# Optimization experiments

Measured on AMD Instinct MI355X. Metric: run time of the kernel, lower is better.

## Reference

```python
import jax, jax.numpy as jnp
import numpy as np

EPS = 1e-8
TAU = 0.2
IOU_THR = 0.5
NEG = -1e9
N, C, H, D_FG, D_CLS = 8192, 1024, 256, 64, 128


def setup_inputs() -> dict:
    key = jax.random.key(0)
    ks = jax.random.split(key, 11)
    def lin(k, fan_in, fan_out):
        return jax.random.normal(k, (fan_in, fan_out), jnp.float32) / np.sqrt(fan_in)
    return {
        "roi_feats": jax.random.normal(ks[0], (N, C), jnp.float32),
        "labels": jax.random.randint(ks[1], (N,), 0, 21, jnp.int32).astype(jnp.int64),
        "ious": jax.random.uniform(ks[2], (N,), jnp.float32),
        "fg_w1": lin(ks[3], C, H), "fg_b1": jnp.zeros((H,), jnp.float32),
        "fg_w2": lin(ks[4], H, D_FG), "fg_b2": jnp.zeros((D_FG,), jnp.float32),
        "cls_w1": lin(ks[5], C, H), "cls_b1": jnp.zeros((H,), jnp.float32),
        "cls_w2": lin(ks[6], H, D_CLS), "cls_b2": jnp.zeros((D_CLS,), jnp.float32),
    }


def _project_normalize(x, w1, b1, w2, b2):
    h = jax.nn.relu(x @ w1 + b1)
    z = h @ w2 + b2
    norm = jnp.maximum(jnp.linalg.norm(z, axis=1, keepdims=True), EPS)
    return z / norm


def _forward(roi_feats, labels, ious, fg_w1, fg_b1, fg_w2, fg_b2, cls_w1, cls_b1, cls_w2, cls_b2):
    n = roi_feats.shape[0]
    z_fg = _project_normalize(roi_feats, fg_w1, fg_b1, fg_w2, fg_b2)
    z_cls = _project_normalize(roi_feats, cls_w1, cls_b1, cls_w2, cls_b2)

    ignore = labels == -1
    fg = (labels > 0) & ~ignore
    iou_weight = jnp.where(ious > IOU_THR, ious, 0.0)
    eye = jnp.eye(n, dtype=bool)

    # ---- fg/bg contrastive (bg_as_negatives_only=True) ----
    sim_fg = (z_fg @ z_fg.T) / TAU                       # [N,N]
    exp_sim = jnp.exp(sim_fg)
    denom = jnp.sum(exp_sim * (~eye).astype(jnp.float32), axis=1)
    pos = (fg & ~ignore)[None, :] & ~eye                 # positives: fg columns, no self
    n_pos = jnp.sum(pos, axis=1)
    numer = jnp.sum(exp_sim * pos.astype(jnp.float32), axis=1)
    # original computes den = denom + EPS then -log((numer+EPS)/(den+EPS))
    loss_i = -jnp.log((numer + EPS) / (denom + 2.0 * EPS))
    valid = (fg & ~ignore) & (n_pos > 0)
    w = iou_weight * valid.astype(jnp.float32)
    loss_fg_bg = jnp.sum(w * loss_i) / (jnp.sum(w) + EPS)

    # ---- class supervised contrastive ----
    sim_cls = (z_cls @ z_cls.T) / TAU
    sim_masked = jnp.where(eye, NEG, sim_cls)
    log_denom = jax.nn.logsumexp(sim_masked, axis=1)     # [N]
    log_p = jnp.where(eye, NEG, sim_cls - log_denom[:, None])
    # pos_mask keeps diagonal (as in original): same label, col not ignore, col label != 0
    posc = (labels[None, :] == labels[:, None]) & (~ignore)[None, :] & (labels[None, :] != 0)
    n_posc = jnp.sum(posc, axis=1).astype(jnp.float32)
    sum_log_p = jnp.sum(log_p * posc.astype(jnp.float32), axis=1)
    valid_c = (fg & ~ignore) & (n_posc > 0) & jnp.isfinite(log_denom)
    Lzi = jnp.where(valid_c, -sum_log_p / (n_posc + EPS), 0.0)
    wc = iou_weight * valid_c.astype(jnp.float32)
    loss_supcon = jnp.sum(wc * Lzi) / (jnp.sum(wc) + EPS)

    return jnp.stack([loss_fg_bg, loss_supcon])


def reference(roi_feats, labels, ious, fg_w1, fg_b1, fg_w2, fg_b2, cls_w1, cls_b1, cls_w2, cls_b2):
    return _forward(roi_feats, labels, ious, fg_w1, fg_b1, fg_w2, fg_b2, cls_w1, cls_b1, cls_w2, cls_b2)
```

## Files before the change

kernel.cpp:

```cpp
#include <hip/hip_runtime.h>


typedef __attribute__((ext_vector_type(8))) short bs8;
typedef __attribute__((ext_vector_type(4))) float f4;

#define MFMA_BF16(a, b, c) __builtin_amdgcn_mfma_f32_16x16x32_bf16((a), (b), (c), 0, 0, 0)

#if defined(__has_builtin)
#if __has_builtin(__builtin_amdgcn_exp2f)
#define EXP2F(x) __builtin_amdgcn_exp2f(x)
#endif
#endif
#ifndef EXP2F
#define EXP2F(x) exp2f(x)
#endif

#define K_LOG2E 7.2134752044448170f

__device__ __forceinline__ unsigned short f2bf(float f) {
  unsigned int u = __float_as_uint(f);
  u = (u + 0x7fffu + ((u >> 16) & 1u)) >> 16;
  return (unsigned short)u;
}
__device__ __forceinline__ float bf2f(unsigned short s) {
  return __uint_as_float(((unsigned int)s) << 16);
}

constexpr size_t O_W1T  = 0;
constexpr size_t O_W2TF = 1048576;
constexpr size_t O_W2TC = 1081344;
constexpr size_t O_H    = 1146880;
constexpr size_t O_ZF   = 9535488;
constexpr size_t O_ZC   = 10584064;
constexpr size_t O_SCLS = 12681216;
constexpr size_t O_ROWD = 12697600;
constexpr size_t O_ROWN = 12730368;
constexpr size_t O_ROWS = 12763136;
constexpr size_t O_SCAL = 12795904;
constexpr size_t O_HIST = 12795920;
constexpr size_t O_NFG  = 12796048;
constexpr size_t O_CNT  = O_SCLS + 31 * 128 * 4;
constexpr int ZERO_WORDS = (int)((O_SCAL + 16 - O_SCLS) / 4);

__global__ void __launch_bounds__(256) prep_kernel(
    const float* __restrict__ fgw1, const float* __restrict__ clsw1,
    const float* __restrict__ fgw2, const float* __restrict__ clsw2,
    const int* __restrict__ labels,
    unsigned short* __restrict__ W1T, unsigned short* __restrict__ W2Tf,
    unsigned short* __restrict__ W2Tc,
    int* __restrict__ hist, int* __restrict__ nfg, float* __restrict__ zp) {
  const int b = blockIdx.x;
  const int t = threadIdx.x;

  if (b >= 141) {
    const int i = (b - 141) * 256 + t;
    if (i < ZERO_WORDS) zp[i] = 0.f;
    return;
  }
  if (b == 140) {
    __shared__ int sh[33];
    if (t < 33) sh[t] = 0;
    __syncthreads();
    for (int it = 0; it < 32; it++) {
      const int lab = labels[it * 256 + t];
      if (lab >= 0 && lab < 32) atomicAdd(&sh[lab], 1);
      if (lab > 0) atomicAdd(&sh[32], 1);
    }
    __syncthreads();
    if (t < 32) hist[t] = sh[t];
    if (t == 32) *nfg = sh[32];
    return;
  }
  int m, tb;
  if (b < 64)       { m = 0; tb = b; }
  else if (b < 128) { m = 1; tb = b - 64; }
  else if (b < 132) { m = 2; tb = b - 128; }
  else              { m = 3; tb = b - 132; }
  __shared__ float tile[64][65];
  const float* src;
  unsigned short* dst;
  int R, C;
  if (m == 0)      { src = fgw1;  dst = W1T;              R = 1024; C = 256; }
  else if (m == 1) { src = clsw1; dst = W1T + 256 * 1024; R = 1024; C = 256; }
  else if (m == 2) { src = fgw2;  dst = W2Tf;             R = 256;  C = 64;  }
  else             { src = clsw2; dst = W2Tc;             R = 256;  C = 128; }
  const int cT = C >> 6;
  const int r0 = (tb / cT) << 6, c0 = (tb % cT) << 6;
  {
    const int rr = t >> 4, cc = (t & 15) << 2;
#pragma unroll
    for (int i = 0; i < 4; i++) {
      float4 v = *(const float4*)(src + (size_t)(r0 + rr + i * 16) * C + c0 + cc);
      tile[rr + i * 16][cc] = v.x; tile[rr + i * 16][cc + 1] = v.y;
      tile[rr + i * 16][cc + 2] = v.z; tile[rr + i * 16][cc + 3] = v.w;
    }
  }
  __syncthreads();
  {
    const int dr = t >> 2, dc = (t & 3) << 4;
    bs8 o0, o1;
#pragma unroll
    for (int j = 0; j < 8; j++) o0[j] = (short)f2bf(tile[dc + j][dr]);
#pragma unroll
    for (int j = 0; j < 8; j++) o1[j] = (short)f2bf(tile[dc + 8 + j][dr]);
    unsigned short* dp = dst + (size_t)(c0 + dr) * R + r0 + dc;
    *(bs8*)dp = o0;
    *(bs8*)(dp + 8) = o1;
  }
}

__global__ void __launch_bounds__(512) gemm1_kernel(
    const float* __restrict__ X, const unsigned short* __restrict__ W1T,
    const float* __restrict__ b1f, const float* __restrict__ b1c,
    unsigned short* __restrict__ H) {
  __shared__ __align__(16) unsigned short lA[64 * 72];
  __shared__ __align__(16) unsigned short lB[128 * 72];
  const int t = threadIdx.x;
  const int w = t >> 6, lane = t & 63, ln = lane & 15, quad = lane >> 4;
  const int wr = (w & 3) * 16, wc = (w >> 2) * 64;
  const int m0 = blockIdx.x * 64, n0 = blockIdx.y * 128;

  const int ar = t >> 3, ac = (t & 7) * 8;
  const int br = t >> 2, bc = (t & 3) * 16;
  const float* xbase = X + (size_t)(m0 + ar) * 1024 + ac;
  const unsigned short* bbase = W1T + (size_t)(n0 + br) * 1024 + bc;

  float4 xa[2];
  bs8 xb[2];
#pragma unroll
  for (int i = 0; i < 2; i++) xa[i] = *(const float4*)(xbase + i * 4);
#pragma unroll
  for (int i = 0; i < 2; i++) xb[i] = *(const bs8*)(bbase + i * 8);

  f4 acc[4];
#pragma unroll
  for (int s = 0; s < 4; s++) acc[s] = (f4){0.f, 0.f, 0.f, 0.f};

  for (int ks = 0; ks < 16; ks++) {
    {
      bs8 av;
      av[0] = (short)f2bf(xa[0].x); av[1] = (short)f2bf(xa[0].y);
      av[2] = (short)f2bf(xa[0].z); av[3] = (short)f2bf(xa[0].w);
      av[4] = (short)f2bf(xa[1].x); av[5] = (short)f2bf(xa[1].y);
      av[6] = (short)f2bf(xa[1].z); av[7] = (short)f2bf(xa[1].w);
      *(bs8*)&lA[ar * 72 + ac] = av;
      unsigned short* bp = &lB[br * 72 + bc];
      *(bs8*)(bp) = xb[0];
      *(bs8*)(bp + 8) = xb[1];
    }
    __syncthreads();
    if (ks < 15) {
      const int k1 = (ks + 1) * 64;
#pragma unroll
      for (int i = 0; i < 2; i++) xa[i] = *(const float4*)(xbase + k1 + i * 4);
#pragma unroll
      for (int i = 0; i < 2; i++) xb[i] = *(const bs8*)(bbase + k1 + i * 8);
    }
#pragma unroll
    for (int kk = 0; kk < 2; kk++) {
      bs8 af = *(const bs8*)&lA[(wr + ln) * 72 + kk * 32 + quad * 8];
#pragma unroll
      for (int s = 0; s < 4; s++) {
        bs8 bf = *(const bs8*)&lB[(wc + s * 16 + ln) * 72 + kk * 32 + quad * 8];
        acc[s] = MFMA_BF16(af, bf, acc[s]);
      }
    }
    __syncthreads();
  }
#pragma unroll
  for (int s = 0; s < 4; s++) {
    const int n = n0 + wc + s * 16 + ln;
    const float b = (n < 256) ? b1f[n] : b1c[n - 256];
#pragma unroll
    for (int r = 0; r < 4; r++) {
      float v = fmaxf(acc[s][r] + b, 0.f);
      H[(size_t)(m0 + wr + quad * 4 + r) * 512 + n] = f2bf(v);
    }
  }
}

__global__ void __launch_bounds__(256) gemm2_kernel(
    const unsigned short* __restrict__ H,
    const unsigned short* __restrict__ W2Tf, const unsigned short* __restrict__ W2Tc,
    const float* __restrict__ b2f, const float* __restrict__ b2c,
    const int* __restrict__ labels,
    unsigned short* __restrict__ Zf, unsigned short* __restrict__ Zc,
    float* __restrict__ Scls) {
  __shared__ float sS[21 * 128];
  const int t = threadIdx.x;
  for (int i = t; i < 21 * 128; i += 256) sS[i] = 0.f;
  __syncthreads();

  const int w = t >> 6, lane = t & 63, ln = lane & 15, quad = lane >> 4;
  const int rw = blockIdx.x * 32 + (w & 1) * 16;

  if (w < 2) {
    const unsigned short* hrow = H + (size_t)(rw + ln) * 512;
    f4 acc[4];
#pragma unroll
    for (int s = 0; s < 4; s++) acc[s] = (f4){0.f, 0.f, 0.f, 0.f};
#pragma unroll
    for (int ks = 0; ks < 8; ks++) {
      bs8 af = *(const bs8*)(hrow + ks * 32 + quad * 8);
#pragma unroll
      for (int s = 0; s < 4; s++) {
        bs8 bf = *(const bs8*)(W2Tf + (size_t)(s * 16 + ln) * 256 + ks * 32 + quad * 8);
        acc[s] = MFMA_BF16(af, bf, acc[s]);
      }
    }
    float ss[4] = {0.f, 0.f, 0.f, 0.f};
#pragma unroll
    for (int s = 0; s < 4; s++) {
      float b = b2f[s * 16 + ln];
#pragma unroll
      for (int r = 0; r < 4; r++) {
        acc[s][r] += b;
        ss[r] = fmaf(acc[s][r], acc[s][r], ss[r]);
      }
    }
#pragma unroll
    for (int r = 0; r < 4; r++) {
#pragma unroll
      for (int off = 1; off < 16; off <<= 1) ss[r] += __shfl_xor(ss[r], off, 64);
      float sc = 1.f / fmaxf(sqrtf(ss[r]), 1e-8f);
#pragma unroll
      for (int s = 0; s < 4; s++)
        Zf[(size_t)(rw + quad * 4 + r) * 64 + s * 16 + ln] = f2bf(acc[s][r] * sc);
    }
  } else {
    const unsigned short* hrow = H + (size_t)(rw + ln) * 512 + 256;
    f4 acc[8];
#pragma unroll
    for (int s = 0; s < 8; s++) acc[s] = (f4){0.f, 0.f, 0.f, 0.f};
#pragma unroll
    for (int ks = 0; ks < 8; ks++) {
      bs8 af = *(const bs8*)(hrow + ks * 32 + quad * 8);
#pragma unroll
      for (int s = 0; s < 8; s++) {
        bs8 bf = *(const bs8*)(W2Tc + (size_t)(s * 16 + ln) * 256 + ks * 32 + quad * 8);
        acc[s] = MFMA_BF16(af, bf, acc[s]);
      }
    }
    float ss[4] = {0.f, 0.f, 0.f, 0.f};
#pragma unroll
    for (int s = 0; s < 8; s++) {
      float b = b2c[s * 16 + ln];
#pragma unroll
      for (int r = 0; r < 4; r++) {
        acc[s][r] += b;
        ss[r] = fmaf(acc[s][r], acc[s][r], ss[r]);
      }
    }
#pragma unroll
    for (int r = 0; r < 4; r++) {
#pragma unroll
      for (int off = 1; off < 16; off <<= 1) ss[r] += __shfl_xor(ss[r], off, 64);
      float sc = 1.f / fmaxf(sqrtf(ss[r]), 1e-8f);
      const int lab = labels[rw + quad * 4 + r];
#pragma unroll
      for (int s = 0; s < 8; s++) {
        const unsigned short us = f2bf(acc[s][r] * sc);
        Zc[(size_t)(rw + quad * 4 + r) * 128 + s * 16 + ln] = us;
        if (lab > 0 && lab < 21) atomicAdd(&sS[lab * 128 + s * 16 + ln], bf2f(us));
      }
    }
  }

  __syncthreads();
  for (int i = t; i < 20 * 128; i += 256) {
    const float v = sS[128 + i];
    if (v != 0.f) atomicAdd(&Scls[128 + i], v);
  }
}

__global__ void __launch_bounds__(256) sim2_kernel(
    const unsigned short* __restrict__ Zf, const unsigned short* __restrict__ Zc,
    const int* __restrict__ labels,
    float* __restrict__ rowD, float* __restrict__ rowN, float* __restrict__ rowS) {
  const int bi = blockIdx.x, y = blockIdx.y;
  const bool isfg = (y < 9);
  const int y2 = isfg ? y : y - 9;
  int dlo, dhi;
  if (y2 == 0)      { dlo = 0;      dhi = 3;      }
  else if (y2 < 8)  { dlo = y2 * 4; dhi = y2 * 4 + 3; }
  else              { dlo = 32;     dhi = 32; if (bi >= 32) return; }

  __shared__ __align__(16) char arena[19456];
  const int t = threadIdx.x;
  const int w = t >> 6, lane = t & 63, ln = lane & 15, quad = lane >> 4;
  const int rbase = bi * 128 + w * 32;

  if (isfg) {
    unsigned short* sZf = (unsigned short*)arena;
    float* sFg = (float*)(arena + 9216);
    float* sCol = (float*)(arena + 9472);

    bs8 afg[2][2];
    float fgr[2][4];
#pragma unroll
    for (int rs = 0; rs < 2; rs++) {
      const unsigned short* zf = Zf + (size_t)(rbase + rs * 16 + ln) * 64;
#pragma unroll
      for (int s = 0; s < 2; s++) afg[rs][s] = *(const bs8*)(zf + s * 32 + quad * 8);
#pragma unroll
      for (int r = 0; r < 4; r++)
        fgr[rs][r] = (labels[rbase + rs * 16 + quad * 4 + r] > 0) ? 1.f : 0.f;
    }

    float dacc[2][4] = {}, nacc[2][4] = {};

    for (int d = dlo; d <= dhi; d++) {
      const int bj = (bi + d) & 63;
      float cd[2][4] = {}, cn[2][4] = {};

#pragma unroll
      for (int ct = 0; ct < 2; ct++) {
        const int c0 = bj * 128 + ct * 64;
        __syncthreads();
#pragma unroll
        for (int i = 0; i < 2; i++) {
          int ch = t + i * 256;
          int j = ch >> 3, c8 = (ch & 7) * 8;
          *(bs8*)&sZf[j * 72 + c8] = *(const bs8*)(Zf + (size_t)(c0 + j) * 64 + c8);
        }
        if (t < 64) sFg[t] = (labels[c0 + t] > 0) ? 1.f : 0.f;
        __syncthreads();

#pragma unroll
        for (int s = 0; s < 4; s++) {
          const int lcol = s * 16 + ln;
          const float fgc = sFg[lcol];
          bs8 b0 = *(const bs8*)&sZf[lcol * 72 + quad * 8];
          bs8 b1 = *(const bs8*)&sZf[lcol * 72 + 32 + quad * 8];
#pragma unroll
          for (int rs = 0; rs < 2; rs++) {
            f4 c = {0.f, 0.f, 0.f, 0.f};
            c = MFMA_BF16(afg[rs][0], b0, c);
            c = MFMA_BF16(afg[rs][1], b1, c);
#pragma unroll
            for (int r = 0; r < 4; r++) {
              float e = EXP2F(c[r] * K_LOG2E);
              dacc[rs][r] += e;
              nacc[rs][r] = fmaf(fgc, e, nacc[rs][r]);
              cd[ct][s] += e;
              cn[ct][s] = fmaf(fgr[rs][r], e, cn[ct][s]);
            }
          }
        }
      }

      if (d != 0) {
#pragma unroll
        for (int ct = 0; ct < 2; ct++)
#pragma unroll
          for (int s = 0; s < 4; s++) {
            float dv = cd[ct][s], nv = cn[ct][s];
#pragma unroll
            for (int off = 16; off < 64; off <<= 1) {
              dv += __shfl_xor(dv, off, 64);
              nv += __shfl_xor(nv, off, 64);
            }
            if (quad == 0) {
              const int idx = (((w * 2 + ct) * 4 + s) * 16 + ln) * 2;
              sCol[idx] = dv;
              sCol[idx + 1] = nv;
            }
          }
        __syncthreads();
        if (t < 128) {
          const int ct = t >> 6, s = (t >> 4) & 3, lm = t & 15;
          float dv = 0.f, nv = 0.f;
#pragma unroll
          for (int ww = 0; ww < 4; ww++) {
            const int idx = (((ww * 2 + ct) * 4 + s) * 16 + lm) * 2;
            dv += sCol[idx];
            nv += sCol[idx + 1];
          }
          const int col = bj * 128 + t;
          atomicAdd(&rowD[col], dv);
          atomicAdd(&rowN[col], nv);
        }
      }
    }

#pragma unroll
    for (int rs = 0; rs < 2; rs++)
#pragma unroll
      for (int r = 0; r < 4; r++) {
        float dv = dacc[rs][r], nv = nacc[rs][r];
#pragma unroll
        for (int off = 1; off < 16; off <<= 1) {
          dv += __shfl_xor(dv, off, 64);
          nv += __shfl_xor(nv, off, 64);
        }
        if (ln == 0) {
          int row = rbase + rs * 16 + quad * 4 + r;
          atomicAdd(&rowD[row], dv);
          atomicAdd(&rowN[row], nv);
        }
      }
  } else {
    unsigned short* sZc = (unsigned short*)arena;
    float* sCol = (float*)(arena + 17408);

    bs8 acl[2][4];
#pragma unroll
    for (int rs = 0; rs < 2; rs++) {
      const unsigned short* zc = Zc + (size_t)(rbase + rs * 16 + ln) * 128;
#pragma unroll
      for (int s = 0; s < 4; s++) acl[rs][s] = *(const bs8*)(zc + s * 32 + quad * 8);
    }

    float sacc[2][4] = {};

    for (int d = dlo; d <= dhi; d++) {
      const int bj = (bi + d) & 63;
      float cs[2][4] = {};

#pragma unroll
      for (int ct = 0; ct < 2; ct++) {
        const int c0 = bj * 128 + ct * 64;
        __syncthreads();
#pragma unroll
        for (int i = 0; i < 4; i++) {
          int ch = t + i * 256;
          int j = ch >> 4, c8 = (ch & 15) * 8;
          *(bs8*)&sZc[j * 136 + c8] = *(const bs8*)(Zc + (size_t)(c0 + j) * 128 + c8);
        }
        __syncthreads();

#pragma unroll
        for (int s = 0; s < 4; s++) {
          const int lcol = s * 16 + ln;
          bs8 bc0 = *(const bs8*)&sZc[lcol * 136 + quad * 8];
          bs8 bc1 = *(const bs8*)&sZc[lcol * 136 + 32 + quad * 8];
          bs8 bc2 = *(const bs8*)&sZc[lcol * 136 + 64 + quad * 8];
          bs8 bc3 = *(const bs8*)&sZc[lcol * 136 + 96 + quad * 8];
#pragma unroll
          for (int rs = 0; rs < 2; rs++) {
            f4 c = {0.f, 0.f, 0.f, 0.f};
            c = MFMA_BF16(acl[rs][0], bc0, c);
            c = MFMA_BF16(acl[rs][1], bc1, c);
            c = MFMA_BF16(acl[rs][2], bc2, c);
            c = MFMA_BF16(acl[rs][3], bc3, c);
#pragma unroll
            for (int r = 0; r < 4; r++) {
              float e = EXP2F(c[r] * K_LOG2E);
              sacc[rs][r] += e;
              cs[ct][s] += e;
            }
          }
        }
      }

      if (d != 0) {
#pragma unroll
        for (int ct = 0; ct < 2; ct++)
#pragma unroll
          for (int s = 0; s < 4; s++) {
            float sv = cs[ct][s];
#pragma unroll
            for (int off = 16; off < 64; off <<= 1) sv += __shfl_xor(sv, off, 64);
            if (quad == 0) sCol[((w * 2 + ct) * 4 + s) * 16 + ln] = sv;
          }
        __syncthreads();
        if (t < 128) {
          const int ct = t >> 6, s = (t >> 4) & 3, lm = t & 15;
          float sv = 0.f;
#pragma unroll
          for (int ww = 0; ww < 4; ww++) sv += sCol[((ww * 2 + ct) * 4 + s) * 16 + lm];
          atomicAdd(&rowS[bj * 128 + t], sv);
        }
      }
    }

#pragma unroll
    for (int rs = 0; rs < 2; rs++)
#pragma unroll
      for (int r = 0; r < 4; r++) {
        float sv = sacc[rs][r];
#pragma unroll
        for (int off = 1; off < 16; off <<= 1) sv += __shfl_xor(sv, off, 64);
        if (ln == 0)
          atomicAdd(&rowS[rbase + rs * 16 + quad * 4 + r], sv);
      }
  }
}

__global__ void __launch_bounds__(256) finalize_kernel(
    const unsigned short* __restrict__ Zf, const unsigned short* __restrict__ Zc,
    const int* __restrict__ labels, const float* __restrict__ ious,
    const float* __restrict__ rowD, const float* __restrict__ rowN,
    const float* __restrict__ rowS, const float* __restrict__ Scls,
    const int* __restrict__ hist, const int* __restrict__ nfg,
    float* __restrict__ scal, unsigned int* __restrict__ cnt,
    float* __restrict__ out) {
  __shared__ float red[4][4];
  const int t = threadIdx.x, w = t >> 6, lane = t & 63;
  float aw0 = 0.f, al0 = 0.f, aw1 = 0.f, al1 = 0.f;
  const int NFG = *nfg;
  for (int it = 0; it < 16; it++) {
    const int i = it * 512 + blockIdx.x * 4 + w;
    const int lab = labels[i];
    if (lab > 0 && lab < 32) {
      const float iou = ious[i];
      const float iw = (iou > 0.5f) ? iou : 0.f;
      float dot = 0.f, ssq = 0.f;
#pragma unroll
      for (int p = 0; p < 2; p++) {
        const int k = lane + p * 64;
        const float z = bf2f(Zc[(size_t)i * 128 + k]);
        dot = fmaf(z, Scls[lab * 128 + k], dot);
        ssq = fmaf(z, z, ssq);
      }
      float zf = bf2f(Zf[(size_t)i * 64 + lane]);
      float ssqf = zf * zf;
#pragma unroll
      for (int off = 1; off < 64; off <<= 1) {
        dot += __shfl_xor(dot, off, 64);
        ssq += __shfl_xor(ssq, off, 64);
        ssqf += __shfl_xor(ssqf, off, 64);
      }
      if (lane == 0) {
        const float ef = EXP2F(K_LOG2E * ssqf);
        if (NFG - 1 > 0) {
          const float D = rowD[i] - ef;
          const float Nn = rowN[i] - ef;
          const float loss = logf(D + 2e-8f) - logf(Nn + 1e-8f);
          aw0 += iw;
          al0 += iw * loss;
        }
        const int npc = hist[lab];
        if (npc > 0) {
          const float S = rowS[i] - EXP2F(K_LOG2E * ssq);
          const float logden = logf(S);
          const float slp = (dot - ssq) * 5.0f - (float)(npc - 1) * logden - 1e9f;
          aw1 += iw;
          al1 += iw * (-slp / ((float)npc + 1e-8f));
        }
      }
    }
  }
  if (lane == 0) { red[w][0] = aw0; red[w][1] = al0; red[w][2] = aw1; red[w][3] = al1; }
  __syncthreads();
  if (t < 4) atomicAdd(&scal[t], red[0][t] + red[1][t] + red[2][t] + red[3][t]);
  __syncthreads();
  if (t == 0) {
    __threadfence();
    const unsigned int ticket = atomicAdd(cnt, 1u);
    if (ticket == gridDim.x - 1) {
      __threadfence();
      const float s0 = atomicAdd(&scal[0], 0.f);
      const float s1 = atomicAdd(&scal[1], 0.f);
      const float s2 = atomicAdd(&scal[2], 0.f);
      const float s3 = atomicAdd(&scal[3], 0.f);
      out[0] = s1 / (s0 + 1e-8f);
      out[1] = s3 / (s2 + 1e-8f);
    }
  }
}

extern "C" void kernel_launch(void* const* d_in, const int* in_sizes, int n_in,
                              void* d_out, int out_size, void* d_ws, size_t ws_size,
                              hipStream_t stream) {
  (void)in_sizes; (void)n_in; (void)out_size; (void)ws_size;
  const float* roi    = (const float*)d_in[0];
  const int*   labels = (const int*)d_in[1];
  const float* ious   = (const float*)d_in[2];
  const float* fgw1   = (const float*)d_in[3];
  const float* fgb1   = (const float*)d_in[4];
  const float* fgw2   = (const float*)d_in[5];
  const float* fgb2   = (const float*)d_in[6];
  const float* clsw1  = (const float*)d_in[7];
  const float* clsb1  = (const float*)d_in[8];
  const float* clsw2  = (const float*)d_in[9];
  const float* clsb2  = (const float*)d_in[10];

  char* ws = (char*)d_ws;
  unsigned short* W1T  = (unsigned short*)(ws + O_W1T);
  unsigned short* W2Tf = (unsigned short*)(ws + O_W2TF);
  unsigned short* W2Tc = (unsigned short*)(ws + O_W2TC);
  unsigned short* Hb   = (unsigned short*)(ws + O_H);
  unsigned short* Zf   = (unsigned short*)(ws + O_ZF);
  unsigned short* Zc   = (unsigned short*)(ws + O_ZC);
  float* Scls = (float*)(ws + O_SCLS);
  float* rowD = (float*)(ws + O_ROWD);
  float* rowN = (float*)(ws + O_ROWN);
  float* rowS = (float*)(ws + O_ROWS);
  float* scal = (float*)(ws + O_SCAL);
  unsigned int* cnt = (unsigned int*)(ws + O_CNT);
  int* hist = (int*)(ws + O_HIST);
  int* nfg  = (int*)(ws + O_NFG);
  float* out = (float*)d_out;

  hipLaunchKernelGGL(prep_kernel, dim3(254), dim3(256), 0, stream,
                     fgw1, clsw1, fgw2, clsw2, labels, W1T, W2Tf, W2Tc,
                     hist, nfg, (float*)(ws + O_SCLS));
  hipLaunchKernelGGL(gemm1_kernel, dim3(128, 4), dim3(512), 0, stream,
                     roi, W1T, fgb1, clsb1, Hb);
  hipLaunchKernelGGL(gemm2_kernel, dim3(256), dim3(256), 0, stream,
                     Hb, W2Tf, W2Tc, fgb2, clsb2, labels, Zf, Zc, Scls);
  hipLaunchKernelGGL(sim2_kernel, dim3(64, 18), dim3(256), 0, stream,
                     Zf, Zc, labels, rowD, rowN, rowS);
  hipLaunchKernelGGL(finalize_kernel, dim3(128), dim3(256), 0, stream,
                     Zf, Zc, labels, ious, rowD, rowN, rowS, Scls, hist, nfg,
                     scal, cnt, out);
}
```

Measured before the change: 201.6 us.

## Fuse fg and class similarity passes into one sim2 block per tile pair

Result: slower. 224.8 us (+11.5%).

```diff
diff --git a/kernel.cpp b/kernel.cpp
--- a/kernel.cpp
+++ b/kernel.cpp
@@ -278,213 +278,154 @@
     const int* __restrict__ labels,
     float* __restrict__ rowD, float* __restrict__ rowN, float* __restrict__ rowS) {
   const int bi = blockIdx.x, y = blockIdx.y;
-  const bool isfg = (y < 9);
-  const int y2 = isfg ? y : y - 9;
   int dlo, dhi;
-  if (y2 == 0)      { dlo = 0;      dhi = 3;      }
-  else if (y2 < 8)  { dlo = y2 * 4; dhi = y2 * 4 + 3; }
-  else              { dlo = 32;     dhi = 32; if (bi >= 32) return; }
-
-  __shared__ __align__(16) char arena[19456];
+  if (y < 16) { dlo = 2 * y; dhi = 2 * y + 1; }
+  else        { dlo = 32;    dhi = 32; if (bi >= 32) return; }
+
+  __shared__ __align__(16) unsigned short sZf[64 * 72];
+  __shared__ __align__(16) unsigned short sZc[64 * 136];
+  __shared__ float sFg[64];
+  __shared__ float sCol[4][2][4][16][3];
   const int t = threadIdx.x;
   const int w = t >> 6, lane = t & 63, ln = lane & 15, quad = lane >> 4;
   const int rbase = bi * 128 + w * 32;
 
-  if (isfg) {
-    unsigned short* sZf = (unsigned short*)arena;
-    float* sFg = (float*)(arena + 9216);
-    float* sCol = (float*)(arena + 9472);
-
-    bs8 afg[2][2];
-    float fgr[2][4];
-#pragma unroll
-    for (int rs = 0; rs < 2; rs++) {
-      const unsigned short* zf = Zf + (size_t)(rbase + rs * 16 + ln) * 64;
-#pragma unroll
-      for (int s = 0; s < 2; s++) afg[rs][s] = *(const bs8*)(zf + s * 32 + quad * 8);
-#pragma unroll
-      for (int r = 0; r < 4; r++)
-        fgr[rs][r] = (labels[rbase + rs * 16 + quad * 4 + r] > 0) ? 1.f : 0.f;
-    }
-
-    float dacc[2][4] = {}, nacc[2][4] = {};
-
-    for (int d = dlo; d <= dhi; d++) {
-      const int bj = (bi + d) & 63;
-      float cd[2][4] = {}, cn[2][4] = {};
-
-#pragma unroll
-      for (int ct = 0; ct < 2; ct++) {
-        const int c0 = bj * 128 + ct * 64;
-        __syncthreads();
-#pragma unroll
-        for (int i = 0; i < 2; i++) {
-          int ch = t + i * 256;
-          int j = ch >> 3, c8 = (ch & 7) * 8;
-          *(bs8*)&sZf[j * 72 + c8] = *(const bs8*)(Zf + (size_t)(c0 + j) * 64 + c8);
-        }
-        if (t < 64) sFg[t] = (labels[c0 + t] > 0) ? 1.f : 0.f;
-        __syncthreads();
-
-#pragma unroll
-        for (int s = 0; s < 4; s++) {
-          const int lcol = s * 16 + ln;
-          const float fgc = sFg[lcol];
-          bs8 b0 = *(const bs8*)&sZf[lcol * 72 + quad * 8];
-          bs8 b1 = *(const bs8*)&sZf[lcol * 72 + 32 + quad * 8];
-#pragma unroll
-          for (int rs = 0; rs < 2; rs++) {
-            f4 c = {0.f, 0.f, 0.f, 0.f};
-            c = MFMA_BF16(afg[rs][0], b0, c);
-            c = MFMA_BF16(afg[rs][1], b1, c);
-#pragma unroll
-            for (int r = 0; r < 4; r++) {
-              float e = EXP2F(c[r] * K_LOG2E);
-              dacc[rs][r] += e;
-              nacc[rs][r] = fmaf(fgc, e, nacc[rs][r]);
-              cd[ct][s] += e;
-              cn[ct][s] = fmaf(fgr[rs][r], e, cn[ct][s]);
-            }
+  bs8 afg[2][2], acl[2][4];
+  float fgr[2][4];
+#pragma unroll
+  for (int rs = 0; rs < 2; rs++) {
+    const unsigned short* zf = Zf + (size_t)(rbase + rs * 16 + ln) * 64;
+    const unsigned short* zc = Zc + (size_t)(rbase + rs * 16 + ln) * 128;
+#pragma unroll
+    for (int s = 0; s < 2; s++) afg[rs][s] = *(const bs8*)(zf + s * 32 + quad * 8);
+#pragma unroll
+    for (int s = 0; s < 4; s++) acl[rs][s] = *(const bs8*)(zc + s * 32 + quad * 8);
+#pragma unroll
+    for (int r = 0; r < 4; r++)
+      fgr[rs][r] = (labels[rbase + rs * 16 + quad * 4 + r] > 0) ? 1.f : 0.f;
+  }
+
+  float dacc[2][4] = {}, nacc[2][4] = {}, sacc[2][4] = {};
+
+  for (int d = dlo; d <= dhi; d++) {
+    const int bj = (bi + d) & 63;
+    float cd[2][4] = {}, cn[2][4] = {}, cs[2][4] = {};
+
+#pragma unroll
+    for (int ct = 0; ct < 2; ct++) {
+      const int c0 = bj * 128 + ct * 64;
+      __syncthreads();
+#pragma unroll
+      for (int i = 0; i < 2; i++) {
+        int ch = t + i * 256;
+        int j = ch >> 3, c8 = (ch & 7) * 8;
+        *(bs8*)&sZf[j * 72 + c8] = *(const bs8*)(Zf + (size_t)(c0 + j) * 64 + c8);
+      }
+#pragma unroll
+      for (int i = 0; i < 4; i++) {
+        int ch = t + i * 256;
+        int j = ch >> 4, c8 = (ch & 15) * 8;
+        *(bs8*)&sZc[j * 136 + c8] = *(const bs8*)(Zc + (size_t)(c0 + j) * 128 + c8);
+      }
+      if (t < 64) sFg[t] = (labels[c0 + t] > 0) ? 1.f : 0.f;
+      __syncthreads();
+
+#pragma unroll
+      for (int s = 0; s < 4; s++) {
+        const int lcol = s * 16 + ln;
+        const float fgc = sFg[lcol];
+        bs8 b0 = *(const bs8*)&sZf[lcol * 72 + quad * 8];
+        bs8 b1 = *(const bs8*)&sZf[lcol * 72 + 32 + quad * 8];
+#pragma unroll
+        for (int rs = 0; rs < 2; rs++) {
+          f4 c = {0.f, 0.f, 0.f, 0.f};
+          c = MFMA_BF16(afg[rs][0], b0, c);
+          c = MFMA_BF16(afg[rs][1], b1, c);
+#pragma unroll
+          for (int r = 0; r < 4; r++) {
+            float e = EXP2F(c[r] * K_LOG2E);
+            dacc[rs][r] += e;
+            nacc[rs][r] = fmaf(fgc, e, nacc[rs][r]);
+            cd[ct][s] += e;
+            cn[ct][s] = fmaf(fgr[rs][r], e, cn[ct][s]);
           }
         }
-      }
-
-      if (d != 0) {
-#pragma unroll
-        for (int ct = 0; ct < 2; ct++)
-#pragma unroll
-          for (int s = 0; s < 4; s++) {
-            float dv = cd[ct][s], nv = cn[ct][s];
-#pragma unroll
-            for (int off = 16; off < 64; off <<= 1) {
-              dv += __shfl_xor(dv, off, 64);
-              nv += __shfl_xor(nv, off, 64);
-            }
-            if (quad == 0) {
-              const int idx = (((w * 2 + ct) * 4 + s) * 16 + ln) * 2;
-              sCol[idx] = dv;
-              sCol[idx + 1] = nv;
-            }
-          }
-        __syncthreads();
-        if (t < 128) {
-          const int ct = t >> 6, s = (t >> 4) & 3, lm = t & 15;
-          float dv = 0.f, nv = 0.f;
-#pragma unroll
-          for (int ww = 0; ww < 4; ww++) {
-            const int idx = (((ww * 2 + ct) * 4 + s) * 16 + lm) * 2;
-            dv += sCol[idx];
-            nv += sCol[idx + 1];
-          }
-          const int col = bj * 128 + t;
-          atomicAdd(&rowD[col], dv);
-          atomicAdd(&rowN[col], nv);
-        }
-      }
-    }
-
-#pragma unroll
-    for (int rs = 0; rs < 2; rs++)
-#pragma unroll
-      for (int r = 0; r < 4; r++) {
-        float dv = dacc[rs][r], nv = nacc[rs][r];
-#pragma unroll
-        for (int off = 1; off < 16; off <<= 1) {
-          dv += __shfl_xor(dv, off, 64);
-          nv += __shfl_xor(nv, off, 64);
-        }
-        if (ln == 0) {
-          int row = rbase + rs * 16 + quad * 4 + r;
-          atomicAdd(&rowD[row], dv);
-          atomicAdd(&rowN[row], nv);
-        }
-      }
-  } else {
-    unsigned short* sZc = (unsigned short*)arena;
-    float* sCol = (float*)(arena + 17408);
-
-    bs8 acl[2][4];
-#pragma unroll
-    for (int rs = 0; rs < 2; rs++) {
-      const unsigned short* zc = Zc + (size_t)(rbase + rs * 16 + ln) * 128;
-#pragma unroll
-      for (int s = 0; s < 4; s++) acl[rs][s] = *(const bs8*)(zc + s * 32 + quad * 8);
-    }
-
-    float sacc[2][4] = {};
-
-    for (int d = dlo; d <= dhi; d++) {
-      const int bj = (bi + d) & 63;
-      float cs[2][4] = {};
-
-#pragma unroll
-      for (int ct = 0; ct < 2; ct++) {
-        const int c0 = bj * 128 + ct * 64;
-        __syncthreads();
-#pragma unroll
-        for (int i = 0; i < 4; i++) {
-          int ch = t + i * 256;
-          int j = ch >> 4, c8 = (ch & 15) * 8;
-          *(bs8*)&sZc[j * 136 + c8] = *(const bs8*)(Zc + (size_t)(c0 + j) * 128 + c8);
-        }
-        __syncthreads();
-
-#pragma unroll
-        for (int s = 0; s < 4; s++) {
-          const int lcol = s * 16 + ln;
-          bs8 bc0 = *(const bs8*)&sZc[lcol * 136 + quad * 8];
-          bs8 bc1 = *(const bs8*)&sZc[lcol * 136 + 32 + quad * 8];
-          bs8 bc2 = *(const bs8*)&sZc[lcol * 136 + 64 + quad * 8];
-          bs8 bc3 = *(const bs8*)&sZc[lcol * 136 + 96 + quad * 8];
-#pragma unroll
-          for (int rs = 0; rs < 2; rs++) {
-            f4 c = {0.f, 0.f, 0.f, 0.f};
-            c = MFMA_BF16(acl[rs][0], bc0, c);
-            c = MFMA_BF16(acl[rs][1], bc1, c);
-            c = MFMA_BF16(acl[rs][2], bc2, c);
-            c = MFMA_BF16(acl[rs][3], bc3, c);
-#pragma unroll
-            for (int r = 0; r < 4; r++) {
-              float e = EXP2F(c[r] * K_LOG2E);
-              sacc[rs][r] += e;
-              cs[ct][s] += e;
-            }
+        bs8 bc0 = *(const bs8*)&sZc[lcol * 136 + quad * 8];
+        bs8 bc1 = *(const bs8*)&sZc[lcol * 136 + 32 + quad * 8];
+        bs8 bc2 = *(const bs8*)&sZc[lcol * 136 + 64 + quad * 8];
+        bs8 bc3 = *(const bs8*)&sZc[lcol * 136 + 96 + quad * 8];
+#pragma unroll
+        for (int rs = 0; rs < 2; rs++) {
+          f4 c = {0.f, 0.f, 0.f, 0.f};
+          c = MFMA_BF16(acl[rs][0], bc0, c);
+          c = MFMA_BF16(acl[rs][1], bc1, c);
+          c = MFMA_BF16(acl[rs][2], bc2, c);
+          c = MFMA_BF16(acl[rs][3], bc3, c);
+#pragma unroll
+          for (int r = 0; r < 4; r++) {
+            float e = EXP2F(c[r] * K_LOG2E);
+            sacc[rs][r] += e;
+            cs[ct][s] += e;
           }
         }
       }
-
-      if (d != 0) {
-#pragma unroll
-        for (int ct = 0; ct < 2; ct++)
-#pragma unroll
-          for (int s = 0; s < 4; s++) {
-            float sv = cs[ct][s];
-#pragma unroll
-            for (int off = 16; off < 64; off <<= 1) sv += __shfl_xor(sv, off, 64);
-            if (quad == 0) sCol[((w * 2 + ct) * 4 + s) * 16 + ln] = sv;
+    }
+
+    if (d != 0) {
+      __syncthreads();
+#pragma unroll
+      for (int ct = 0; ct < 2; ct++)
+#pragma unroll
+        for (int s = 0; s < 4; s++) {
+          float dv = cd[ct][s], nv = cn[ct][s], sv = cs[ct][s];
+#pragma unroll
+          for (int off = 16; off < 64; off <<= 1) {
+            dv += __shfl_xor(dv, off, 64);
+            nv += __shfl_xor(nv, off, 64);
+            sv += __shfl_xor(sv, off, 64);
           }
-        __syncthreads();
-        if (t < 128) {
-          const int ct = t >> 6, s = (t >> 4) & 3, lm = t & 15;
-          float sv = 0.f;
-#pragma unroll
-          for (int ww = 0; ww < 4; ww++) sv += sCol[((ww * 2 + ct) * 4 + s) * 16 + lm];
-          atomicAdd(&rowS[bj * 128 + t], sv);
+          if (quad == 0) {
+            sCol[w][ct][s][ln][0] = dv;
+            sCol[w][ct][s][ln][1] = nv;
+            sCol[w][ct][s][ln][2] = sv;
+          }
         }
-      }
-    }
-
-#pragma unroll
-    for (int rs = 0; rs < 2; rs++)
-#pragma unroll
-      for (int r = 0; r < 4; r++) {
-        float sv = sacc[rs][r];
-#pragma unroll
-        for (int off = 1; off < 16; off <<= 1) sv += __shfl_xor(sv, off, 64);
-        if (ln == 0)
-          atomicAdd(&rowS[rbase + rs * 16 + quad * 4 + r], sv);
-      }
-  }
+      __syncthreads();
+      if (t < 128) {
+        const int ct = t >> 6, s = (t >> 4) & 3, lm = t & 15;
+        float dv = 0.f, nv = 0.f, sv = 0.f;
+#pragma unroll
+        for (int ww = 0; ww < 4; ww++) {
+          dv += sCol[ww][ct][s][lm][0];
+          nv += sCol[ww][ct][s][lm][1];
+          sv += sCol[ww][ct][s][lm][2];
+        }
+        const int col = bj * 128 + t;
+        atomicAdd(&rowD[col], dv);
+        atomicAdd(&rowN[col], nv);
+        atomicAdd(&rowS[col], sv);
+      }
+    }
+  }
+
+#pragma unroll
+  for (int rs = 0; rs < 2; rs++)
+#pragma unroll
+    for (int r = 0; r < 4; r++) {
+      float dv = dacc[rs][r], nv = nacc[rs][r], sv = sacc[rs][r];
+#pragma unroll
+      for (int off = 1; off < 16; off <<= 1) {
+        dv += __shfl_xor(dv, off, 64);
+        nv += __shfl_xor(nv, off, 64);
+        sv += __shfl_xor(sv, off, 64);
+      }
+      if (ln == 0) {
+        int row = rbase + rs * 16 + quad * 4 + r;
+        atomicAdd(&rowD[row], dv);
+        atomicAdd(&rowN[row], nv);
+        atomicAdd(&rowS[row], sv);
+      }
+    }
 }
 
 __global__ void __launch_bounds__(256) finalize_kernel(
@@ -600,7 +541,7 @@
                      roi, W1T, fgb1, clsb1, Hb);
   hipLaunchKernelGGL(gemm2_kernel, dim3(256), dim3(256), 0, stream,
                      Hb, W2Tf, W2Tc, fgb2, clsb2, labels, Zf, Zc, Scls);
-  hipLaunchKernelGGL(sim2_kernel, dim3(64, 18), dim3(256), 0, stream,
+  hipLaunchKernelGGL(sim2_kernel, dim3(64, 17), dim3(256), 0, stream,
                      Zf, Zc, labels, rowD, rowN, rowS);
   hipLaunchKernelGGL(finalize_kernel, dim3(128), dim3(256), 0, stream,
                      Zf, Zc, labels, ious, rowD, rowN, rowS, Scls, hist, nfg,
```
